# Kernel tuning notes

Hardware: AMD Instinct MI355X
Metric: run time of the kernel (lower is better)

The kernel has to match this reference:

```python
import jax, jax.numpy as jnp
import numpy as np

BATCH = 16384
IN_DIM = 256
UNITS = 256


def setup_inputs() -> dict:
    key = jax.random.key(0)
    ks = jax.random.split(key, 5)
    scale = 1.0 / np.sqrt(IN_DIM + UNITS)
    return {
        "x": jax.random.normal(ks[0], (BATCH, IN_DIM), dtype=jnp.float32),
        "prev_h": jax.random.normal(ks[1], (BATCH, UNITS), dtype=jnp.float32),
        "Wz": jax.random.normal(ks[2], (IN_DIM + UNITS, UNITS), dtype=jnp.float32) * scale,
        "bz": jnp.zeros((UNITS,), dtype=jnp.float32),
        "Wr": jax.random.normal(ks[3], (IN_DIM + UNITS, UNITS), dtype=jnp.float32) * scale,
        "br": jnp.zeros((UNITS,), dtype=jnp.float32),
        "Ws": jax.random.normal(ks[4], (IN_DIM + UNITS, UNITS), dtype=jnp.float32) * scale,
        "bs": jnp.zeros((UNITS,), dtype=jnp.float32),
    }


def reference(x, prev_h, Wz, bz, Wr, br, Ws, bs):
    # concat order matches the TF module: [prev_h, x]
    concat = jnp.concatenate([prev_h, x], axis=1)  # [B, units+in_dim]
    z = jax.nn.sigmoid(concat @ Wz + bz)
    r = jax.nn.sigmoid(concat @ Wr + br)
    concat_cand = jnp.concatenate([r * prev_h, x], axis=1)
    h_tilda = jnp.tanh(concat_cand @ Ws + bs)
    h_new = (1.0 - z) * prev_h + z * h_tilda
    return h_new
```

## Files before the change

### kernel.cpp

```cpp
#include <hip/hip_runtime.h>
#include <hip/hip_bf16.h>


#define ROWS 64

typedef float f32x4 __attribute__((ext_vector_type(4)));
typedef __bf16 bf16x8 __attribute__((ext_vector_type(8)));
typedef unsigned short us8 __attribute__((ext_vector_type(8)));
typedef unsigned short us4v __attribute__((ext_vector_type(4)));

static __device__ __forceinline__ unsigned short f2bf(float f) {
    __bf16 h = (__bf16)f;
    return __builtin_bit_cast(unsigned short, h);
}
static __device__ __forceinline__ float bf2f(unsigned short u) {
    union { unsigned u; float f; } v; v.u = ((unsigned)u) << 16;
    return v.f;
}

__global__ void pack_weights(const float* __restrict__ Wz,
                             const float* __restrict__ Wr,
                             const float* __restrict__ Ws,
                             unsigned short* __restrict__ out) {
    int gid = blockIdx.x * blockDim.x + threadIdx.x;
    int w    = gid >> 14;
    int rem  = gid & 16383;
    int kt   = rem >> 10;
    int rem2 = rem & 1023;
    int nt   = rem2 >> 6;
    int lane = rem2 & 63;
    int hi = lane >> 4, lo = lane & 15;
    const float* W = (w == 0) ? Wz : (w == 1) ? Wr : Ws;
    const float* src = W + (size_t)(kt * 32 + hi * 8) * 256 + nt * 16 + lo;
    us8 o;
#pragma unroll
    for (int j = 0; j < 8; ++j) o[j] = f2bf(src[(size_t)j * 256]);
    *(us8*)&out[(size_t)w * 131072 + (size_t)(((kt * 16 + nt) * 64 + lane) * 8)] = o;
}

__launch_bounds__(1024, 4)
__global__ void gru_main(const float* __restrict__ x,
                         const float* __restrict__ ph,
                         const float* __restrict__ bz,
                         const float* __restrict__ br,
                         const float* __restrict__ bs,
                         const unsigned short* __restrict__ Wp,
                         float* __restrict__ out) {
    __shared__ unsigned short sm[ROWS * 512];
    __shared__ unsigned short rh[ROWS * 256];

    const int tid  = threadIdx.x;
    const int lane = tid & 63;
    const int wid  = tid >> 6;
    const int brow = blockIdx.x * ROWS;

    const int l15 = lane & 15;
    const int kg  = (lane >> 4) << 3;
    const int col = wid * 16 + l15;

    const unsigned short* pz = Wp          + (size_t)((wid * 64 + lane) * 8);
    const unsigned short* pr = Wp + 131072 + (size_t)((wid * 64 + lane) * 8);
    const unsigned short* ps = Wp + 262144 + (size_t)((wid * 64 + lane) * 8);
    us8 b0n = *(const us8*)pz;
    us8 b1n = *(const us8*)pr;
    float bzc = bz[col], brc = br[col], bsc = bs[col];

#pragma unroll
    for (int it = 0; it < 4; ++it) {
        int i   = tid + it * 1024;
        int row = i >> 6;
        int c4  = (i & 63) << 2;
        int swr = (row & 7) << 3;
        float4 a = *(const float4*)&ph[(size_t)(brow + row) * 256 + c4];
        us4v u; u.x = f2bf(a.x); u.y = f2bf(a.y); u.z = f2bf(a.z); u.w = f2bf(a.w);
        *(us4v*)&sm[row * 512 + (c4 ^ swr)] = u;
    }
    __syncthreads();

    float4 xr[4];
#pragma unroll
    for (int it = 0; it < 4; ++it) {
        int i   = tid + it * 1024;
        int row = i >> 6;
        int c4  = (i & 63) << 2;
        xr[it] = *(const float4*)&x[(size_t)(brow + row) * 256 + c4];
    }

    f32x4 accz[4] = {};
    f32x4 accr[4] = {};
#pragma unroll 4
    for (int kt = 0; kt < 8; ++kt) {
        bf16x8 B0 = __builtin_bit_cast(bf16x8, b0n);
        bf16x8 B1 = __builtin_bit_cast(bf16x8, b1n);
        b0n = *(const us8*)(pz + (size_t)(kt + 1) * 8192);
        b1n = *(const us8*)(pr + (size_t)(kt + 1) * 8192);
        int ak = kt * 32 + kg;
#pragma unroll
        for (int m = 0; m < 4; ++m) {
            int arow = m * 16 + l15;
            bf16x8 a = __builtin_bit_cast(bf16x8,
                *(const us8*)&sm[arow * 512 + (ak ^ ((arow & 7) << 3))]);
            accz[m] = __builtin_amdgcn_mfma_f32_16x16x32_bf16(a, B0, accz[m], 0, 0, 0);
            accr[m] = __builtin_amdgcn_mfma_f32_16x16x32_bf16(a, B1, accr[m], 0, 0, 0);
        }
    }

#pragma unroll
    for (int it = 0; it < 4; ++it) {
        int i   = tid + it * 1024;
        int row = i >> 6;
        int c4  = (i & 63) << 2;
        int swr = (row & 7) << 3;
        us4v v; v.x = f2bf(xr[it].x); v.y = f2bf(xr[it].y);
        v.z = f2bf(xr[it].z); v.w = f2bf(xr[it].w);
        *(us4v*)&sm[row * 512 + ((256 + c4) ^ swr)] = v;
    }
    __syncthreads();

    us8 s0n = *(const us8*)(ps + (size_t)8 * 8192);
    us8 s1n = *(const us8*)(ps + (size_t)9 * 8192);

    f32x4 accs[4] = {};
#pragma unroll 4
    for (int kt = 8; kt < 16; ++kt) {
        bf16x8 B0 = __builtin_bit_cast(bf16x8, b0n);
        bf16x8 B1 = __builtin_bit_cast(bf16x8, b1n);
        bf16x8 S  = __builtin_bit_cast(bf16x8, s0n);
        s0n = s1n;
        if (kt < 15) {
            size_t no = (size_t)(kt + 1) * 8192;
            b0n = *(const us8*)(pz + no);
            b1n = *(const us8*)(pr + no);
        }
        if (kt < 14) s1n = *(const us8*)(ps + (size_t)(kt + 2) * 8192);
        int ak = kt * 32 + kg;
#pragma unroll
        for (int m = 0; m < 4; ++m) {
            int arow = m * 16 + l15;
            bf16x8 a = __builtin_bit_cast(bf16x8,
                *(const us8*)&sm[arow * 512 + (ak ^ ((arow & 7) << 3))]);
            accz[m] = __builtin_amdgcn_mfma_f32_16x16x32_bf16(a, B0, accz[m], 0, 0, 0);
            accr[m] = __builtin_amdgcn_mfma_f32_16x16x32_bf16(a, B1, accr[m], 0, 0, 0);
            accs[m] = __builtin_amdgcn_mfma_f32_16x16x32_bf16(a, S,  accs[m], 0, 0, 0);
        }
    }

    s0n = *(const us8*)ps;
    s1n = *(const us8*)(ps + 8192);

    float pst[4][4];
    const int rrow0 = (lane >> 4) * 4;
#pragma unroll
    for (int m = 0; m < 4; ++m) {
#pragma unroll
        for (int i = 0; i < 4; ++i) {
            int lrow = m * 16 + rrow0 + i;
            int cs = col ^ ((lrow & 7) << 3);
            float p = bf2f(sm[lrow * 512 + cs]);
            float z = 1.f / (1.f + __expf(-(accz[m][i] + bzc)));
            float r = 1.f / (1.f + __expf(-(accr[m][i] + brc)));
            accz[m][i] = z;
            pst[m][i]  = p;
            rh[lrow * 256 + cs] = f2bf(r * p);
        }
    }
    __syncthreads();

#pragma unroll 4
    for (int kt = 0; kt < 8; ++kt) {
        bf16x8 B = __builtin_bit_cast(bf16x8, s0n);
        s0n = s1n;
        if (kt < 6) s1n = *(const us8*)(ps + (size_t)(kt + 2) * 8192);
        int ak = kt * 32 + kg;
#pragma unroll
        for (int m = 0; m < 4; ++m) {
            int arow = m * 16 + l15;
            bf16x8 a = __builtin_bit_cast(bf16x8,
                *(const us8*)&rh[arow * 256 + (ak ^ ((arow & 7) << 3))]);
            accs[m] = __builtin_amdgcn_mfma_f32_16x16x32_bf16(a, B, accs[m], 0, 0, 0);
        }
    }

#pragma unroll
    for (int m = 0; m < 4; ++m) {
#pragma unroll
        for (int i = 0; i < 4; ++i) {
            float s = accs[m][i] + bsc;
            float e = __expf(-2.f * fabsf(s));
            float th = (1.f - e) / (1.f + e);
            th = (s < 0.f) ? -th : th;
            float z = accz[m][i];
            float p = pst[m][i];
            int grow = brow + m * 16 + rrow0 + i;
            out[(size_t)grow * 256 + col] = (1.f - z) * p + z * th;
        }
    }
}

extern "C" void kernel_launch(void* const* d_in, const int* in_sizes, int n_in,
                              void* d_out, int out_size, void* d_ws, size_t ws_size,
                              hipStream_t stream) {
    const float* x  = (const float*)d_in[0];
    const float* ph = (const float*)d_in[1];
    const float* Wz = (const float*)d_in[2];
    const float* bz = (const float*)d_in[3];
    const float* Wr = (const float*)d_in[4];
    const float* br = (const float*)d_in[5];
    const float* Ws = (const float*)d_in[6];
    const float* bs = (const float*)d_in[7];
    unsigned short* Wp = (unsigned short*)d_ws;

    hipLaunchKernelGGL(pack_weights, dim3(192), dim3(256), 0, stream, Wz, Wr, Ws, Wp);
    hipLaunchKernelGGL(gru_main, dim3(256), dim3(1024), 0, stream,
                       x, ph, bz, br, bs, Wp, (float*)d_out);
}
```

Baseline: 33.80 us.

## Split each block's rows into two half-tiles, prefetching the second during the first

Each block now handles its 64 rows as two sequential 32-row halves with separate shared buffers. The second half's prev_h and x rows are loaded into registers while the first half computes. The aim is to hide global-load latency behind MFMA work and to shrink the live accumulator set. In exchange, the weight fragments are streamed twice per block and each half issues half as many MFMAs per weight load, with more barriers.

```diff
diff --git a/kernel.cpp b/kernel.cpp
--- a/kernel.cpp
+++ b/kernel.cpp
@@ -2,7 +2,7 @@
 #include <hip/hip_bf16.h>
 
 
-#define ROWS 64
+#define TROWS 32
 
 typedef float f32x4 __attribute__((ext_vector_type(4)));
 typedef __bf16 bf16x8 __attribute__((ext_vector_type(8)));
@@ -46,48 +46,47 @@
                          const float* __restrict__ bs,
                          const unsigned short* __restrict__ Wp,
                          float* __restrict__ out) {
-    __shared__ unsigned short sm[ROWS * 512];
-    __shared__ unsigned short rh[ROWS * 256];
+    __shared__ unsigned short smA[TROWS * 512];
+    __shared__ unsigned short smB[TROWS * 512];
+    __shared__ unsigned short rhb[TROWS * 256];
 
     const int tid  = threadIdx.x;
     const int lane = tid & 63;
     const int wid  = tid >> 6;
-    const int brow = blockIdx.x * ROWS;
-
-    const int l15 = lane & 15;
-    const int kg  = (lane >> 4) << 3;
-    const int col = wid * 16 + l15;
+    const int brow0 = blockIdx.x * 64;
+    const int brow1 = brow0 + TROWS;
+
+    const int l15   = lane & 15;
+    const int kg    = (lane >> 4) << 3;
+    const int rrow0 = (lane >> 4) * 4;
+    const int col   = wid * 16 + l15;
 
     const unsigned short* pz = Wp          + (size_t)((wid * 64 + lane) * 8);
     const unsigned short* pr = Wp + 131072 + (size_t)((wid * 64 + lane) * 8);
     const unsigned short* ps = Wp + 262144 + (size_t)((wid * 64 + lane) * 8);
     us8 b0n = *(const us8*)pz;
     us8 b1n = *(const us8*)pr;
-    float bzc = bz[col], brc = br[col], bsc = bs[col];
-
-#pragma unroll
-    for (int it = 0; it < 4; ++it) {
-        int i   = tid + it * 1024;
-        int row = i >> 6;
-        int c4  = (i & 63) << 2;
-        int swr = (row & 7) << 3;
-        float4 a = *(const float4*)&ph[(size_t)(brow + row) * 256 + c4];
-        us4v u; u.x = f2bf(a.x); u.y = f2bf(a.y); u.z = f2bf(a.z); u.w = f2bf(a.w);
-        *(us4v*)&sm[row * 512 + (c4 ^ swr)] = u;
-    }
-    __syncthreads();
-
-    float4 xr[4];
-#pragma unroll
-    for (int it = 0; it < 4; ++it) {
-        int i   = tid + it * 1024;
-        int row = i >> 6;
-        int c4  = (i & 63) << 2;
-        xr[it] = *(const float4*)&x[(size_t)(brow + row) * 256 + c4];
-    }
-
-    f32x4 accz[4] = {};
-    f32x4 accr[4] = {};
+    const float bzc = bz[col], brc = br[col], bsc = bs[col];
+
+    float4 p0[2], x0[2];
+#pragma unroll
+    for (int it = 0; it < 2; ++it) {
+        int i = tid + it * 1024;
+        int row = i >> 6, c4 = (i & 63) << 2;
+        p0[it] = *(const float4*)&ph[(size_t)(brow0 + row) * 256 + c4];
+        x0[it] = *(const float4*)&x [(size_t)(brow0 + row) * 256 + c4];
+    }
+#pragma unroll
+    for (int it = 0; it < 2; ++it) {
+        int i = tid + it * 1024;
+        int row = i >> 6, c4 = (i & 63) << 2, swr = (row & 7) << 3;
+        us4v u; u.x = f2bf(p0[it].x); u.y = f2bf(p0[it].y);
+        u.z = f2bf(p0[it].z); u.w = f2bf(p0[it].w);
+        *(us4v*)&smA[row * 512 + (c4 ^ swr)] = u;
+    }
+    __syncthreads();
+
+    f32x4 az[2] = {}, ar[2] = {};
 #pragma unroll 4
     for (int kt = 0; kt < 8; ++kt) {
         bf16x8 B0 = __builtin_bit_cast(bf16x8, b0n);
@@ -96,31 +95,37 @@
         b1n = *(const us8*)(pr + (size_t)(kt + 1) * 8192);
         int ak = kt * 32 + kg;
 #pragma unroll
-        for (int m = 0; m < 4; ++m) {
-            int arow = m * 16 + l15;
-            bf16x8 a = __builtin_bit_cast(bf16x8,
-                *(const us8*)&sm[arow * 512 + (ak ^ ((arow & 7) << 3))]);
-            accz[m] = __builtin_amdgcn_mfma_f32_16x16x32_bf16(a, B0, accz[m], 0, 0, 0);
-            accr[m] = __builtin_amdgcn_mfma_f32_16x16x32_bf16(a, B1, accr[m], 0, 0, 0);
-        }
-    }
-
-#pragma unroll
-    for (int it = 0; it < 4; ++it) {
-        int i   = tid + it * 1024;
-        int row = i >> 6;
-        int c4  = (i & 63) << 2;
-        int swr = (row & 7) << 3;
-        us4v v; v.x = f2bf(xr[it].x); v.y = f2bf(xr[it].y);
-        v.z = f2bf(xr[it].z); v.w = f2bf(xr[it].w);
-        *(us4v*)&sm[row * 512 + ((256 + c4) ^ swr)] = v;
-    }
-    __syncthreads();
+        for (int m = 0; m < 2; ++m) {
+            int arow = m * 16 + l15;
+            bf16x8 a = __builtin_bit_cast(bf16x8,
+                *(const us8*)&smA[arow * 512 + (ak ^ ((arow & 7) << 3))]);
+            az[m] = __builtin_amdgcn_mfma_f32_16x16x32_bf16(a, B0, az[m], 0, 0, 0);
+            ar[m] = __builtin_amdgcn_mfma_f32_16x16x32_bf16(a, B1, ar[m], 0, 0, 0);
+        }
+    }
+#pragma unroll
+    for (int it = 0; it < 2; ++it) {
+        int i = tid + it * 1024;
+        int row = i >> 6, c4 = (i & 63) << 2, swr = (row & 7) << 3;
+        us4v v; v.x = f2bf(x0[it].x); v.y = f2bf(x0[it].y);
+        v.z = f2bf(x0[it].z); v.w = f2bf(x0[it].w);
+        *(us4v*)&smA[row * 512 + ((256 + c4) ^ swr)] = v;
+    }
+    __syncthreads();
+
+    float4 p1[2], x1[2];
+#pragma unroll
+    for (int it = 0; it < 2; ++it) {
+        int i = tid + it * 1024;
+        int row = i >> 6, c4 = (i & 63) << 2;
+        p1[it] = *(const float4*)&ph[(size_t)(brow1 + row) * 256 + c4];
+        x1[it] = *(const float4*)&x [(size_t)(brow1 + row) * 256 + c4];
+    }
 
     us8 s0n = *(const us8*)(ps + (size_t)8 * 8192);
     us8 s1n = *(const us8*)(ps + (size_t)9 * 8192);
 
-    f32x4 accs[4] = {};
+    f32x4 as_[2] = {};
 #pragma unroll 4
     for (int kt = 8; kt < 16; ++kt) {
         bf16x8 B0 = __builtin_bit_cast(bf16x8, b0n);
@@ -135,66 +140,176 @@
         if (kt < 14) s1n = *(const us8*)(ps + (size_t)(kt + 2) * 8192);
         int ak = kt * 32 + kg;
 #pragma unroll
-        for (int m = 0; m < 4; ++m) {
-            int arow = m * 16 + l15;
-            bf16x8 a = __builtin_bit_cast(bf16x8,
-                *(const us8*)&sm[arow * 512 + (ak ^ ((arow & 7) << 3))]);
-            accz[m] = __builtin_amdgcn_mfma_f32_16x16x32_bf16(a, B0, accz[m], 0, 0, 0);
-            accr[m] = __builtin_amdgcn_mfma_f32_16x16x32_bf16(a, B1, accr[m], 0, 0, 0);
-            accs[m] = __builtin_amdgcn_mfma_f32_16x16x32_bf16(a, S,  accs[m], 0, 0, 0);
-        }
-    }
-
+        for (int m = 0; m < 2; ++m) {
+            int arow = m * 16 + l15;
+            bf16x8 a = __builtin_bit_cast(bf16x8,
+                *(const us8*)&smA[arow * 512 + (ak ^ ((arow & 7) << 3))]);
+            az[m] = __builtin_amdgcn_mfma_f32_16x16x32_bf16(a, B0, az[m], 0, 0, 0);
+            ar[m] = __builtin_amdgcn_mfma_f32_16x16x32_bf16(a, B1, ar[m], 0, 0, 0);
+            as_[m] = __builtin_amdgcn_mfma_f32_16x16x32_bf16(a, S,  as_[m], 0, 0, 0);
+        }
+    }
+
+    b0n = *(const us8*)pz;
+    b1n = *(const us8*)pr;
     s0n = *(const us8*)ps;
     s1n = *(const us8*)(ps + 8192);
 
-    float pst[4][4];
-    const int rrow0 = (lane >> 4) * 4;
-#pragma unroll
-    for (int m = 0; m < 4; ++m) {
+    float pst[2][4];
+#pragma unroll
+    for (int m = 0; m < 2; ++m)
 #pragma unroll
         for (int i = 0; i < 4; ++i) {
             int lrow = m * 16 + rrow0 + i;
             int cs = col ^ ((lrow & 7) << 3);
-            float p = bf2f(sm[lrow * 512 + cs]);
-            float z = 1.f / (1.f + __expf(-(accz[m][i] + bzc)));
-            float r = 1.f / (1.f + __expf(-(accr[m][i] + brc)));
-            accz[m][i] = z;
-            pst[m][i]  = p;
-            rh[lrow * 256 + cs] = f2bf(r * p);
-        }
-    }
+            float p = bf2f(smA[lrow * 512 + cs]);
+            float z = 1.f / (1.f + __expf(-(az[m][i] + bzc)));
+            float r = 1.f / (1.f + __expf(-(ar[m][i] + brc)));
+            az[m][i] = z;
+            pst[m][i] = p;
+            rhb[lrow * 256 + cs] = f2bf(r * p);
+        }
     __syncthreads();
 
 #pragma unroll 4
     for (int kt = 0; kt < 8; ++kt) {
-        bf16x8 B = __builtin_bit_cast(bf16x8, s0n);
+        bf16x8 S = __builtin_bit_cast(bf16x8, s0n);
         s0n = s1n;
         if (kt < 6) s1n = *(const us8*)(ps + (size_t)(kt + 2) * 8192);
         int ak = kt * 32 + kg;
 #pragma unroll
-        for (int m = 0; m < 4; ++m) {
-            int arow = m * 16 + l15;
-            bf16x8 a = __builtin_bit_cast(bf16x8,
-                *(const us8*)&rh[arow * 256 + (ak ^ ((arow & 7) << 3))]);
-            accs[m] = __builtin_amdgcn_mfma_f32_16x16x32_bf16(a, B, accs[m], 0, 0, 0);
-        }
-    }
-
-#pragma unroll
-    for (int m = 0; m < 4; ++m) {
+        for (int m = 0; m < 2; ++m) {
+            int arow = m * 16 + l15;
+            bf16x8 a = __builtin_bit_cast(bf16x8,
+                *(const us8*)&rhb[arow * 256 + (ak ^ ((arow & 7) << 3))]);
+            as_[m] = __builtin_amdgcn_mfma_f32_16x16x32_bf16(a, S, as_[m], 0, 0, 0);
+        }
+    }
+
+#pragma unroll
+    for (int m = 0; m < 2; ++m)
 #pragma unroll
         for (int i = 0; i < 4; ++i) {
-            float s = accs[m][i] + bsc;
+            float s = as_[m][i] + bsc;
             float e = __expf(-2.f * fabsf(s));
             float th = (1.f - e) / (1.f + e);
             th = (s < 0.f) ? -th : th;
-            float z = accz[m][i];
-            float p = pst[m][i];
-            int grow = brow + m * 16 + rrow0 + i;
-            out[(size_t)grow * 256 + col] = (1.f - z) * p + z * th;
-        }
-    }
+            float z = az[m][i];
+            out[(size_t)(brow0 + m * 16 + rrow0 + i) * 256 + col]
+                = (1.f - z) * pst[m][i] + z * th;
+        }
+
+#pragma unroll
+    for (int it = 0; it < 2; ++it) {
+        int i = tid + it * 1024;
+        int row = i >> 6, c4 = (i & 63) << 2, swr = (row & 7) << 3;
+        us4v u; u.x = f2bf(p1[it].x); u.y = f2bf(p1[it].y);
+        u.z = f2bf(p1[it].z); u.w = f2bf(p1[it].w);
+        *(us4v*)&smB[row * 512 + (c4 ^ swr)] = u;
+    }
+    __syncthreads();
+
+    f32x4 az1[2] = {}, ar1[2] = {};
+#pragma unroll 4
+    for (int kt = 0; kt < 8; ++kt) {
+        bf16x8 B0 = __builtin_bit_cast(bf16x8, b0n);
+        bf16x8 B1 = __builtin_bit_cast(bf16x8, b1n);
+        b0n = *(const us8*)(pz + (size_t)(kt + 1) * 8192);
+        b1n = *(const us8*)(pr + (size_t)(kt + 1) * 8192);
+        int ak = kt * 32 + kg;
+#pragma unroll
+        for (int m = 0; m < 2; ++m) {
+            int arow = m * 16 + l15;
+            bf16x8 a = __builtin_bit_cast(bf16x8,
+                *(const us8*)&smB[arow * 512 + (ak ^ ((arow & 7) << 3))]);
+            az1[m] = __builtin_amdgcn_mfma_f32_16x16x32_bf16(a, B0, az1[m], 0, 0, 0);
+            ar1[m] = __builtin_amdgcn_mfma_f32_16x16x32_bf16(a, B1, ar1[m], 0, 0, 0);
+        }
+    }
+#pragma unroll
+    for (int it = 0; it < 2; ++it) {
+        int i = tid + it * 1024;
+        int row = i >> 6, c4 = (i & 63) << 2, swr = (row & 7) << 3;
+        us4v v; v.x = f2bf(x1[it].x); v.y = f2bf(x1[it].y);
+        v.z = f2bf(x1[it].z); v.w = f2bf(x1[it].w);
+        *(us4v*)&smB[row * 512 + ((256 + c4) ^ swr)] = v;
+    }
+    __syncthreads();
+
+    s0n = *(const us8*)(ps + (size_t)8 * 8192);
+    s1n = *(const us8*)(ps + (size_t)9 * 8192);
+
+    f32x4 as1[2] = {};
+#pragma unroll 4
+    for (int kt = 8; kt < 16; ++kt) {
+        bf16x8 B0 = __builtin_bit_cast(bf16x8, b0n);
+        bf16x8 B1 = __builtin_bit_cast(bf16x8, b1n);
+        bf16x8 S  = __builtin_bit_cast(bf16x8, s0n);
+        s0n = s1n;
+        if (kt < 15) {
+            size_t no = (size_t)(kt + 1) * 8192;
+            b0n = *(const us8*)(pz + no);
+            b1n = *(const us8*)(pr + no);
+        }
+        if (kt < 14) s1n = *(const us8*)(ps + (size_t)(kt + 2) * 8192);
+        int ak = kt * 32 + kg;
+#pragma unroll
+        for (int m = 0; m < 2; ++m) {
+            int arow = m * 16 + l15;
+            bf16x8 a = __builtin_bit_cast(bf16x8,
+                *(const us8*)&smB[arow * 512 + (ak ^ ((arow & 7) << 3))]);
+            az1[m] = __builtin_amdgcn_mfma_f32_16x16x32_bf16(a, B0, az1[m], 0, 0, 0);
+            ar1[m] = __builtin_amdgcn_mfma_f32_16x16x32_bf16(a, B1, ar1[m], 0, 0, 0);
+            as1[m] = __builtin_amdgcn_mfma_f32_16x16x32_bf16(a, S,  as1[m], 0, 0, 0);
+        }
+    }
+
+    s0n = *(const us8*)ps;
+    s1n = *(const us8*)(ps + 8192);
+
+    float pst1[2][4];
+#pragma unroll
+    for (int m = 0; m < 2; ++m)
+#pragma unroll
+        for (int i = 0; i < 4; ++i) {
+            int lrow = m * 16 + rrow0 + i;
+            int cs = col ^ ((lrow & 7) << 3);
+            float p = bf2f(smB[lrow * 512 + cs]);
+            float z = 1.f / (1.f + __expf(-(az1[m][i] + bzc)));
+            float r = 1.f / (1.f + __expf(-(ar1[m][i] + brc)));
+            az1[m][i] = z;
+            pst1[m][i] = p;
+            rhb[lrow * 256 + cs] = f2bf(r * p);
+        }
+    __syncthreads();
+
+#pragma unroll 4
+    for (int kt = 0; kt < 8; ++kt) {
+        bf16x8 S = __builtin_bit_cast(bf16x8, s0n);
+        s0n = s1n;
+        if (kt < 6) s1n = *(const us8*)(ps + (size_t)(kt + 2) * 8192);
+        int ak = kt * 32 + kg;
+#pragma unroll
+        for (int m = 0; m < 2; ++m) {
+            int arow = m * 16 + l15;
+            bf16x8 a = __builtin_bit_cast(bf16x8,
+                *(const us8*)&rhb[arow * 256 + (ak ^ ((arow & 7) << 3))]);
+            as1[m] = __builtin_amdgcn_mfma_f32_16x16x32_bf16(a, S, as1[m], 0, 0, 0);
+        }
+    }
+
+#pragma unroll
+    for (int m = 0; m < 2; ++m)
+#pragma unroll
+        for (int i = 0; i < 4; ++i) {
+            float s = as1[m][i] + bsc;
+            float e = __expf(-2.f * fabsf(s));
+            float th = (1.f - e) / (1.f + e);
+            th = (s < 0.f) ? -th : th;
+            float z = az1[m][i];
+            out[(size_t)(brow1 + m * 16 + rrow0 + i) * 256 + col]
+                = (1.f - z) * pst1[m][i] + z * th;
+        }
 }
 
 extern "C" void kernel_launch(void* const* d_in, const int* in_sizes, int n_in,
```

Measured after the change: 39.05 us. 1.16x slower.
